# Kernel tuning notes

Measured on AMD Instinct MI355X. Metric: run time of the kernel, lower is better.

## Reference

```python
import jax, jax.numpy as jnp
import numpy as np

B, N, F = 1024, 256, 8
E = 1024
OUT = 128          # NNConv out-channels (hardcoded in module)
N_DIV = 64         # len(num_actions)
PER = 3            # actions per diverter
FEAT = N * OUT     # feature_size() = num_nodes * 128


def setup_inputs() -> dict:
    key = jax.random.key(0)
    ks = jax.random.split(key, 20)
    s = lambda *sh: 0.02
    return {
        "x": jax.random.normal(ks[0], (B, N, F), jnp.float32),
        "edge_index": jax.random.randint(ks[1], (2, E), 0, N, jnp.int64),
        # edge-MLP nn1: Linear(1,64) -> ReLU -> Linear(64, F*OUT)
        "w1": jax.random.normal(ks[2], (1, 64), jnp.float32) * 0.1,
        "b1": jnp.zeros((64,), jnp.float32),
        "w2": jax.random.normal(ks[3], (64, F * OUT), jnp.float32) * 0.02,
        "b2": jnp.zeros((F * OUT,), jnp.float32),
        # NNConv root weight + bias
        "root_w": jax.random.normal(ks[4], (F, OUT), jnp.float32) * 0.1,
        "conv_b": jnp.zeros((OUT,), jnp.float32),
        # dueling heads
        "adv_w": jax.random.normal(ks[5], (FEAT, N_DIV * PER), jnp.float32) * 0.005,
        "adv_b": jnp.zeros((N_DIV * PER,), jnp.float32),
        "v1w": jax.random.normal(ks[6], (FEAT, 64), jnp.float32) * 0.005,
        "v1b": jnp.zeros((64,), jnp.float32),
        "v2w": jax.random.normal(ks[7], (64, 64), jnp.float32) * 0.1,
        "v2b": jnp.zeros((64,), jnp.float32),
        "v3w": jax.random.normal(ks[8], (64, N_DIV), jnp.float32) * 0.1,
        "v3b": jnp.zeros((N_DIV,), jnp.float32),
    }


def reference(x, edge_index, w1, b1, w2, b2, root_w, conv_b,
              adv_w, adv_b, v1w, v1b, v2w, v2b, v3w, v3b):
    b, n, f = x.shape
    out_c = root_w.shape[1]
    n_div = v3w.shape[1]
    flat = x.reshape(b * n, f)                              # [B*N, F]
    e = edge_index.shape[1]
    # edge_attr = ones -> edge MLP produces per-edge weight matrix theta
    ea = jnp.ones((e, 1), x.dtype)
    h = jax.nn.relu(ea @ w1 + b1)
    theta = (h @ w2 + b2).reshape(e, f, out_c)              # [E, F, OUT]
    src, tgt = edge_index[0], edge_index[1]
    # gather source feats -> per-edge matmul -> scatter-add at targets
    msg = jnp.einsum('ef,efo->eo', flat[src], theta)        # [E, OUT]
    agg = jnp.zeros((b * n, out_c), x.dtype).at[tgt].add(msg)
    conv = agg + flat @ root_w + conv_b                      # NNConv root + bias
    feat = jax.nn.relu(conv).reshape(b, -1)                  # [B, N*OUT]
    adv = jax.nn.relu(feat @ adv_w + adv_b).reshape(b, n_div, -1)
    val = jax.nn.relu(feat @ v1w + v1b)
    val = jax.nn.relu(val @ v2w + v2b)
    val = val @ v3w + v3b                                    # [B, n_div]
    return val[..., None] + adv - adv.mean(-1, keepdims=True)
```

## Files before the change

kernel.cpp:

```cpp
#include <hip/hip_runtime.h>

#define Bsz 1024
#define Nn 256
#define Fdim 8
#define Eedge 1024
#define OUTC 128
#define CADV 192
#define CTOT 256
#define Ktot 32768
#define ASTR 40
#define XSTR 24

typedef __attribute__((ext_vector_type(8))) short short8;
typedef __attribute__((ext_vector_type(4))) float float4v;

static __device__ inline unsigned short f2bf(float f) {
  union { float f; unsigned u; } v; v.f = f;
  unsigned r = v.u + 0x7FFFu + ((v.u >> 16) & 1u);
  return (unsigned short)(r >> 16);
}
static __device__ inline float bf2f(unsigned short h) {
  union { unsigned u; float f; } v; v.u = ((unsigned)h) << 16;
  return v.f;
}
static __device__ inline uint4 pack8(const unsigned short* b) {
  uint4 v;
  v.x = (unsigned)b[0] | ((unsigned)b[1] << 16);
  v.y = (unsigned)b[2] | ((unsigned)b[3] << 16);
  v.z = (unsigned)b[4] | ((unsigned)b[5] << 16);
  v.w = (unsigned)b[6] | ((unsigned)b[7] << 16);
  return v;
}
static __device__ inline unsigned cvtpk(float a, float b) {
  unsigned r;
  asm("v_cvt_pk_bf16_f32 %0, %1, %2" : "=v"(r) : "v"(a), "v"(b));
  return r;
}
static __device__ inline float hi_of(unsigned p)  {
  union { unsigned u; float f; } v; v.u = p << 16; return v.f;
}
static __device__ inline float hi2_of(unsigned p) {
  union { unsigned u; float f; } v; v.u = p & 0xFFFF0000u; return v.f;
}

__global__ __launch_bounds__(256) void prep_feat_kernel(
    const float* __restrict__ x, const int* __restrict__ ei,
    const float* __restrict__ w1, const float* __restrict__ b1,
    const float* __restrict__ w2, const float* __restrict__ b2,
    const float* __restrict__ rootw, const float* __restrict__ convb,
    const float* __restrict__ advw, const float* __restrict__ v1w,
    unsigned short* __restrict__ wt, unsigned short* __restrict__ feat0)
{
  __shared__ __align__(16) char smem[20480];
  int bid = blockIdx.x, t = threadIdx.x;

  if (bid < 16) {
    float* fs   = (float*)smem;
    float* h_s  = fs;
    float* rw_s = fs + 64;
    float* th_s = fs + 128;
    float* pt_s = fs + 192;
    float* S_s  = fs + 448;
    int*   flag = (int*)(fs + 2496);
    int obase = bid * 8;

    if (t < 64) {
      h_s[t]  = fmaxf(w1[t] + b1[t], 0.f);
      rw_s[t] = rootw[(t >> 3) * OUTC + obase + (t & 7)];
    }
    for (int i = t; i < Nn * Fdim; i += 256) S_s[i] = 0.f;
    if (t == 0) {
      int z = 0;
      for (int i = 1; i < 16; i += 2) z |= ei[i];
      *flag = (z == 0);
    }
    __syncthreads();
    int is64 = *flag;

    {
      int l = t & 63, g = t >> 6;
      int c = (l >> 3) * 128 + obase + (l & 7);
      float p = 0.f;
#pragma unroll
      for (int j = 0; j < 16; ++j)
        p += h_s[g * 16 + j] * w2[(size_t)(g * 16 + j) * 1024 + c];
      pt_s[t] = p;
    }
    int srcs[4], tgts[4];
#pragma unroll
    for (int q = 0; q < 4; ++q) {
      int e = t + q * 256;
      if (is64) { srcs[q] = ei[2 * e]; tgts[q] = ei[2 * (Eedge + e)]; }
      else      { srcs[q] = ei[e];     tgts[q] = ei[Eedge + e]; }
      srcs[q] &= 255; tgts[q] &= 255;
    }
    __syncthreads();
    if (t < 64) {
      int c = (t >> 3) * 128 + obase + (t & 7);
      th_s[t] = b2[c] + pt_s[t] + pt_s[t + 64] + pt_s[t + 128] + pt_s[t + 192];
    }
#pragma unroll
    for (int q = 0; q < 4; ++q) {
      const float* xp = x + srcs[q] * Fdim;
#pragma unroll
      for (int f = 0; f < Fdim; ++f)
        atomicAdd(&S_s[tgts[q] * Fdim + f], xp[f]);
    }
    __syncthreads();
    {
      int n = t;
      const float* xp = x + n * Fdim;
      float4 xa = *(const float4*)xp;
      float4 xb = *(const float4*)(xp + 4);
      float xv[8] = {xa.x, xa.y, xa.z, xa.w, xb.x, xb.y, xb.z, xb.w};
      float sv[8];
#pragma unroll
      for (int f = 0; f < 8; ++f) sv[f] = S_s[n * Fdim + f];
      unsigned short buf[8];
#pragma unroll
      for (int oi = 0; oi < 8; ++oi) {
        float z = convb[obase + oi];
#pragma unroll
        for (int f = 0; f < 8; ++f)
          z += xv[f] * rw_s[f * 8 + oi] + sv[f] * th_s[f * 8 + oi];
        buf[oi] = f2bf(fmaxf(z, 0.f));
      }
      *(uint4*)(feat0 + (size_t)n * OUTC + obase) = pack8(buf);
    }
  } else {
    unsigned short* st = (unsigned short*)smem;
    int kt = bid - 16, c = t;
    const float* src; int stride, col;
    if (c < CADV) { src = advw; stride = CADV; col = c; }
    else          { src = v1w;  stride = 64;   col = c - CADV; }
    float v[32];
#pragma unroll
    for (int i = 0; i < 32; ++i)
      v[i] = src[(size_t)(kt * 32 + i) * stride + col];
    unsigned pk[16];
#pragma unroll
    for (int i = 0; i < 16; ++i) pk[i] = cvtpk(v[2 * i], v[2 * i + 1]);
#pragma unroll
    for (int p = 0; p < 4; ++p) {
      uint4 w4; w4.x = pk[p * 4]; w4.y = pk[p * 4 + 1];
      w4.z = pk[p * 4 + 2]; w4.w = pk[p * 4 + 3];
      *(uint4*)(st + c * ASTR + p * 8) = w4;
    }
    __syncthreads();
    uint4* dst = (uint4*)(wt + (size_t)kt * (CTOT * 32));
    for (int r = 0; r < 4; ++r) {
      int s = r * 256 + c;
      dst[s] = *(const uint4*)(st + (s >> 2) * ASTR + (s & 3) * 8);
    }
  }
}

__global__ __launch_bounds__(512, 2) void gemm_mfma(
    const float* __restrict__ x, const unsigned short* __restrict__ wt,
    const float* __restrict__ rootw, const float* __restrict__ convb,
    const unsigned short* __restrict__ feat0, float* __restrict__ part,
    int iters, int ns)
{
  __shared__ short a_s[2][64 * ASTR];
  __shared__ short b_s[2][256 * ASTR];
  __shared__ short x_s[2][64 * XSTR];
  __shared__ short rw_s[128 * XSTR];
  __shared__ float convb_s[128];
  int t = threadIdx.x;
  int ch = blockIdx.x;
  int mb = blockIdx.y;
  int wave = t >> 6, lane = t & 63;
  int wm = wave >> 2, wn = wave & 3;
  int lm = lane & 15, lq = lane >> 4;

  float4v acc[2][4];
#pragma unroll
  for (int i = 0; i < 2; ++i)
#pragma unroll
    for (int j = 0; j < 4; ++j) acc[i][j] = (float4v)0.f;

  int kt0 = ch * iters;
  int iters4 = iters >> 2;
  int n0 = ch * iters4;
  int wr0 = (t >> 2) * ASTR + (t & 3) * 8;
  int u1 = t + 512;
  int wr1 = (u1 >> 2) * ASTR + (u1 & 3) * 8;
  int grow = (wave & 3) * 16 + lm;
  int gtt  = wave >> 2;

  if (t < 128) {
    float wv[8];
#pragma unroll
    for (int f = 0; f < 8; ++f) wv[f] = rootw[f * OUTC + t];
    unsigned ph[4];
#pragma unroll
    for (int i = 0; i < 4; ++i) ph[i] = cvtpk(wv[2 * i], wv[2 * i + 1]);
    float wl[8];
#pragma unroll
    for (int i = 0; i < 4; ++i) {
      wl[2 * i]     = wv[2 * i]     - hi_of(ph[i]);
      wl[2 * i + 1] = wv[2 * i + 1] - hi2_of(ph[i]);
    }
    unsigned pl[4];
#pragma unroll
    for (int i = 0; i < 4; ++i) pl[i] = cvtpk(wl[2 * i], wl[2 * i + 1]);
    uint4 wh4; wh4.x = ph[0]; wh4.y = ph[1]; wh4.z = ph[2]; wh4.w = ph[3];
    uint4 wl4; wl4.x = pl[0]; wl4.y = pl[1]; wl4.z = pl[2]; wl4.w = pl[3];
    *(uint4*)(rw_s + t * XSTR)     = wh4;
    *(uint4*)(rw_s + t * XSTR + 8) = wl4;
    convb_s[t] = convb[t];
  }
  int xr = (t & 127) >> 1, xh = t & 1;
  const float* xgb = x + ((size_t)(mb * 64 + xr) * Nn) * Fdim + xh * 4;
  if (t < 128) {
    float4 xv = *(const float4*)(xgb + (size_t)n0 * Fdim);
    uint2 dh, dl;
    dh.x = cvtpk(xv.x, xv.y);
    dh.y = cvtpk(xv.z, xv.w);
    dl.x = cvtpk(xv.x - hi_of(dh.x), xv.y - hi2_of(dh.x));
    dl.y = cvtpk(xv.z - hi_of(dh.y), xv.w - hi2_of(dh.y));
    *(uint2*)(x_s[0] + xr * XSTR + xh * 4)     = dh;
    *(uint2*)(x_s[0] + xr * XSTR + 8 + xh * 4) = dl;
  }
  __syncthreads();

  {
    short8 xf = (short8)0;
    if (lq == 0 || lq == 2) xf = *(const short8*)(x_s[0] + grow * XSTR);
    else if (lq == 1)       xf = *(const short8*)(x_s[0] + grow * XSTR + 8);
    int ot = gtt;
    short8 wf = (short8)0;
    if (lq <= 1)      wf = *(const short8*)(rw_s + (ot * 16 + lm) * XSTR);
    else if (lq == 2) wf = *(const short8*)(rw_s + (ot * 16 + lm) * XSTR + 8);
    float4v c = __builtin_amdgcn_mfma_f32_16x16x32_bf16(wf, xf, (float4v)0.f, 0, 0, 0);
    int o0 = ot * 16 + lq * 4;
    float4 cb = *(const float4*)(convb_s + o0);
    unsigned d0 = cvtpk(fmaxf(c[0] + cb.x, 0.f), fmaxf(c[1] + cb.y, 0.f));
    unsigned d1 = cvtpk(fmaxf(c[2] + cb.z, 0.f), fmaxf(c[3] + cb.w, 0.f));
    if (mb == 0 && grow == 0) {
      const unsigned* f0p = (const unsigned*)(feat0 + ((size_t)n0 * OUTC + o0));
      d0 = f0p[0]; d1 = f0p[1];
    }
    uint2 dd; dd.x = d0; dd.y = d1;
    *(uint2*)(a_s[0] + grow * ASTR + gtt * 16 + lq * 4) = dd;
  }

  const uint4* gB = (const uint4*)wt + (size_t)kt0 * 1024;
  uint4 vb0 = gB[t], vb1 = gB[t + 512];
  float4 xpf = {0.f, 0.f, 0.f, 0.f};

  for (int kk = 0; kk < iters; ++kk) {
    int g = kk & 3, grp = kk >> 2;
    short* bb = b_s[kk & 1];
    *(uint4*)(bb + wr0) = vb0;
    *(uint4*)(bb + wr1) = vb1;
    if (g == 0 && grp + 1 < iters4 && t < 128)
      xpf = *(const float4*)(xgb + (size_t)(n0 + grp + 1) * Fdim);
    if (g == 3 && grp + 1 < iters4 && t < 128) {
      uint2 dh, dl;
      dh.x = cvtpk(xpf.x, xpf.y);
      dh.y = cvtpk(xpf.z, xpf.w);
      dl.x = cvtpk(xpf.x - hi_of(dh.x), xpf.y - hi2_of(dh.x));
      dl.y = cvtpk(xpf.z - hi_of(dh.y), xpf.w - hi2_of(dh.y));
      short* xd = x_s[(grp + 1) & 1];
      *(uint2*)(xd + xr * XSTR + xh * 4)     = dh;
      *(uint2*)(xd + xr * XSTR + 8 + xh * 4) = dl;
    }
    if (kk + 1 < iters) {
      const uint4* gB2 = (const uint4*)wt + (size_t)(kt0 + kk + 1) * 1024;
      vb0 = gB2[t]; vb1 = gB2[t + 512];
    }
    __syncthreads();

    short* ab = a_s[kk & 1];
    short8 aF[2];
#pragma unroll
    for (int i = 0; i < 2; ++i)
      aF[i] = *(const short8*)(ab + (wm * 32 + i * 16 + lm) * ASTR + lq * 8);
#pragma unroll
    for (int j = 0; j < 4; ++j) {
      short8 bF = *(const short8*)(bb + (wn * 64 + j * 16 + lm) * ASTR + lq * 8);
#pragma unroll
      for (int i = 0; i < 2; ++i)
        acc[i][j] = __builtin_amdgcn_mfma_f32_16x16x32_bf16(bF, aF[i], acc[i][j], 0, 0, 0);
    }

    if (kk + 1 < iters) {
      int kn = kk + 1;
      int g2 = kn & 3, grp2 = kn >> 2;
      const short* xs = x_s[grp2 & 1];
      int node2 = n0 + grp2;
      short* ad = a_s[kn & 1];
      short8 xf = (short8)0;
      if (lq == 0 || lq == 2) xf = *(const short8*)(xs + grow * XSTR);
      else if (lq == 1)       xf = *(const short8*)(xs + grow * XSTR + 8);
      int ot = g2 * 2 + gtt;
      short8 wf = (short8)0;
      if (lq <= 1)      wf = *(const short8*)(rw_s + (ot * 16 + lm) * XSTR);
      else if (lq == 2) wf = *(const short8*)(rw_s + (ot * 16 + lm) * XSTR + 8);
      float4v c = __builtin_amdgcn_mfma_f32_16x16x32_bf16(wf, xf, (float4v)0.f, 0, 0, 0);
      int o0 = ot * 16 + lq * 4;
      float4 cb = *(const float4*)(convb_s + o0);
      unsigned d0 = cvtpk(fmaxf(c[0] + cb.x, 0.f), fmaxf(c[1] + cb.y, 0.f));
      unsigned d1 = cvtpk(fmaxf(c[2] + cb.z, 0.f), fmaxf(c[3] + cb.w, 0.f));
      if (mb == 0 && grow == 0) {
        const unsigned* f0p = (const unsigned*)(feat0 + ((size_t)node2 * OUTC + o0));
        d0 = f0p[0]; d1 = f0p[1];
      }
      uint2 dd; dd.x = d0; dd.y = d1;
      *(uint2*)(ad + grow * ASTR + gtt * 16 + lq * 4) = dd;
    }
  }

  float* pb = part + ((size_t)(mb * 64) * ns + ch) * CTOT;
#pragma unroll
  for (int i = 0; i < 2; ++i) {
    int m = wm * 32 + i * 16 + lm;
#pragma unroll
    for (int j = 0; j < 4; ++j) {
      int c = wn * 64 + j * 16 + lq * 4;
      *(float4v*)(pb + (size_t)m * ns * CTOT + c) = acc[i][j];
    }
  }
}

__global__ __launch_bounds__(256) void final_kernel(
    const float* __restrict__ part, int ns,
    const float* __restrict__ advb, const float* __restrict__ v1b,
    const float* __restrict__ v2w, const float* __restrict__ v2b,
    const float* __restrict__ v3w, const float* __restrict__ v3b,
    float* __restrict__ out)
{
  __shared__ float4v red_s[4][64];
  __shared__ float adv_s[CADV];
  __shared__ float v1_s[64];
  __shared__ float val2_s[64];
  __shared__ float val3_s[64];
  int b = blockIdx.x, t = threadIdx.x;
  int q = t & 63, r0 = t >> 6;
  const float4v* p4 = (const float4v*)(part + (size_t)b * ns * CTOT);
  float4v s4 = (float4v)0.f;
  for (int i = r0; i < ns; i += 4) s4 += p4[i * 64 + q];
  red_s[r0][q] = s4;
  __syncthreads();
  float s;
  {
    const float* rs = (const float*)red_s;
    s = rs[t] + rs[256 + t] + rs[512 + t] + rs[768 + t];
  }
  if (t < CADV) adv_s[t] = fmaxf(s + advb[t], 0.f);
  else          v1_s[t - CADV] = fmaxf(s + v1b[t - CADV], 0.f);
  __syncthreads();
  if (t < 64) {
    float a = v2b[t];
#pragma unroll
    for (int i = 0; i < 64; ++i) a += v1_s[i] * v2w[i * 64 + t];
    val2_s[t] = fmaxf(a, 0.f);
  }
  __syncthreads();
  if (t < 64) {
    float a = v3b[t];
#pragma unroll
    for (int j = 0; j < 64; ++j) a += val2_s[j] * v3w[j * 64 + t];
    val3_s[t] = a;
  }
  __syncthreads();
  if (t < CADV) {
    int d = t / 3;
    float mean = (adv_s[d * 3] + adv_s[d * 3 + 1] + adv_s[d * 3 + 2]) * (1.f / 3.f);
    out[(size_t)b * CADV + t] = val3_s[d] + adv_s[t] - mean;
  }
}

extern "C" void kernel_launch(void* const* d_in, const int* in_sizes, int n_in,
                              void* d_out, int out_size, void* d_ws, size_t ws_size,
                              hipStream_t stream)
{
  (void)in_sizes; (void)n_in; (void)out_size;
  const float* x     = (const float*)d_in[0];
  const int*   ei    = (const int*)d_in[1];
  const float* w1    = (const float*)d_in[2];
  const float* b1    = (const float*)d_in[3];
  const float* w2    = (const float*)d_in[4];
  const float* b2    = (const float*)d_in[5];
  const float* rootw = (const float*)d_in[6];
  const float* convb = (const float*)d_in[7];
  const float* advw  = (const float*)d_in[8];
  const float* advb  = (const float*)d_in[9];
  const float* v1w   = (const float*)d_in[10];
  const float* v1b   = (const float*)d_in[11];
  const float* v2w   = (const float*)d_in[12];
  const float* v2b   = (const float*)d_in[13];
  const float* v3w   = (const float*)d_in[14];
  const float* v3b   = (const float*)d_in[15];
  float* out = (float*)d_out;

  const size_t f0B = 131072;
  const size_t wtB = (size_t)Ktot * CTOT * 2;

  int NS = 32;
  while (NS > 8 && f0B + wtB + (size_t)NS * Bsz * CTOT * 4 > ws_size)
    NS >>= 1;

  unsigned short* feat0 = (unsigned short*)d_ws;
  unsigned short* wtp   = (unsigned short*)((char*)d_ws + f0B);
  float* part = (float*)((char*)d_ws + f0B + wtB);

  prep_feat_kernel<<<1040, 256, 0, stream>>>(x, ei, w1, b1, w2, b2, rootw,
                                             convb, advw, v1w, wtp, feat0);
  gemm_mfma<<<dim3(NS, 16), 512, 0, stream>>>(x, wtp, rootw, convb, feat0, part,
                                              1024 / NS, NS);
  final_kernel<<<Bsz, 256, 0, stream>>>(part, NS, advb, v1b, v2w, v2b, v3w, v3b, out);
}
```

Measured before the change: 165.5 us.

## Split GEMM output columns across a grid z-dimension and build x fragments in registers

The GEMM's 256 output columns are split into two halves handled by separate blocks (grid z=2). This halves the B tile in shared memory and the accumulators per thread, and launch bounds are raised to 4 blocks per CU for higher occupancy. The x hi/lo bf16 fragments are now built directly in registers from global loads instead of being staged through shared memory. The catch is that the A-side work (x conversion and the root-weight MFMA) is duplicated across the two column halves, and each block does less MFMA work per barrier.

```diff
diff --git a/kernel.cpp b/kernel.cpp
--- a/kernel.cpp
+++ b/kernel.cpp
@@ -19,10 +19,6 @@
   unsigned r = v.u + 0x7FFFu + ((v.u >> 16) & 1u);
   return (unsigned short)(r >> 16);
 }
-static __device__ inline float bf2f(unsigned short h) {
-  union { unsigned u; float f; } v; v.u = ((unsigned)h) << 16;
-  return v.f;
-}
 static __device__ inline uint4 pack8(const unsigned short* b) {
   uint4 v;
   v.x = (unsigned)b[0] | ((unsigned)b[1] << 16);
@@ -41,6 +37,19 @@
 }
 static __device__ inline float hi2_of(unsigned p) {
   union { unsigned u; float f; } v; v.u = p & 0xFFFF0000u; return v.f;
+}
+static __device__ inline short8 make_frag(float4 a, float4 b, int lq) {
+  union { unsigned u[4]; short8 s; } uu;
+  unsigned h0 = cvtpk(a.x, a.y), h1 = cvtpk(a.z, a.w);
+  unsigned h2 = cvtpk(b.x, b.y), h3 = cvtpk(b.z, b.w);
+  uu.u[0] = h0; uu.u[1] = h1; uu.u[2] = h2; uu.u[3] = h3;
+  if (lq == 1) {
+    uu.u[0] = cvtpk(a.x - hi_of(h0), a.y - hi2_of(h0));
+    uu.u[1] = cvtpk(a.z - hi_of(h1), a.w - hi2_of(h1));
+    uu.u[2] = cvtpk(b.x - hi_of(h2), b.y - hi2_of(h2));
+    uu.u[3] = cvtpk(b.z - hi_of(h3), b.w - hi2_of(h3));
+  }
+  return uu.s;
 }
 
 __global__ __launch_bounds__(256) void prep_feat_kernel(
@@ -155,36 +164,34 @@
   }
 }
 
-__global__ __launch_bounds__(512, 2) void gemm_mfma(
+__global__ __launch_bounds__(512, 4) void gemm_mfma(
     const float* __restrict__ x, const unsigned short* __restrict__ wt,
     const float* __restrict__ rootw, const float* __restrict__ convb,
     const unsigned short* __restrict__ feat0, float* __restrict__ part,
     int iters, int ns)
 {
   __shared__ short a_s[2][64 * ASTR];
-  __shared__ short b_s[2][256 * ASTR];
-  __shared__ short x_s[2][64 * XSTR];
+  __shared__ short b_s[2][128 * ASTR];
   __shared__ short rw_s[128 * XSTR];
   __shared__ float convb_s[128];
   int t = threadIdx.x;
   int ch = blockIdx.x;
   int mb = blockIdx.y;
+  int nc = blockIdx.z;
   int wave = t >> 6, lane = t & 63;
   int wm = wave >> 2, wn = wave & 3;
   int lm = lane & 15, lq = lane >> 4;
 
-  float4v acc[2][4];
+  float4v acc[2][2];
 #pragma unroll
   for (int i = 0; i < 2; ++i)
 #pragma unroll
-    for (int j = 0; j < 4; ++j) acc[i][j] = (float4v)0.f;
+    for (int j = 0; j < 2; ++j) acc[i][j] = (float4v)0.f;
 
   int kt0 = ch * iters;
   int iters4 = iters >> 2;
   int n0 = ch * iters4;
   int wr0 = (t >> 2) * ASTR + (t & 3) * 8;
-  int u1 = t + 512;
-  int wr1 = (u1 >> 2) * ASTR + (u1 & 3) * 8;
   int grow = (wave & 3) * 16 + lm;
   int gtt  = wave >> 2;
 
@@ -210,29 +217,24 @@
     *(uint4*)(rw_s + t * XSTR + 8) = wl4;
     convb_s[t] = convb[t];
   }
-  int xr = (t & 127) >> 1, xh = t & 1;
-  const float* xgb = x + ((size_t)(mb * 64 + xr) * Nn) * Fdim + xh * 4;
-  if (t < 128) {
-    float4 xv = *(const float4*)(xgb + (size_t)n0 * Fdim);
-    uint2 dh, dl;
-    dh.x = cvtpk(xv.x, xv.y);
-    dh.y = cvtpk(xv.z, xv.w);
-    dl.x = cvtpk(xv.x - hi_of(dh.x), xv.y - hi2_of(dh.x));
-    dl.y = cvtpk(xv.z - hi_of(dh.y), xv.w - hi2_of(dh.y));
-    *(uint2*)(x_s[0] + xr * XSTR + xh * 4)     = dh;
-    *(uint2*)(x_s[0] + xr * XSTR + 8 + xh * 4) = dl;
+  const float* xrow = x + ((size_t)(mb * 64 + grow) * Nn) * Fdim;
+  float4 xa0 = *(const float4*)(xrow + (size_t)n0 * Fdim);
+  float4 xb0 = *(const float4*)(xrow + (size_t)n0 * Fdim + 4);
+  short8 xf_cur = make_frag(xa0, xb0, lq);
+  short8 xf_next = xf_cur;
+  float4 xpa = xa0, xpb = xb0;
+  if (iters4 > 1) {
+    xpa = *(const float4*)(xrow + (size_t)(n0 + 1) * Fdim);
+    xpb = *(const float4*)(xrow + (size_t)(n0 + 1) * Fdim + 4);
   }
   __syncthreads();
 
   {
-    short8 xf = (short8)0;
-    if (lq == 0 || lq == 2) xf = *(const short8*)(x_s[0] + grow * XSTR);
-    else if (lq == 1)       xf = *(const short8*)(x_s[0] + grow * XSTR + 8);
     int ot = gtt;
     short8 wf = (short8)0;
     if (lq <= 1)      wf = *(const short8*)(rw_s + (ot * 16 + lm) * XSTR);
     else if (lq == 2) wf = *(const short8*)(rw_s + (ot * 16 + lm) * XSTR + 8);
-    float4v c = __builtin_amdgcn_mfma_f32_16x16x32_bf16(wf, xf, (float4v)0.f, 0, 0, 0);
+    float4v c = __builtin_amdgcn_mfma_f32_16x16x32_bf16(wf, xf_cur, (float4v)0.f, 0, 0, 0);
     int o0 = ot * 16 + lq * 4;
     float4 cb = *(const float4*)(convb_s + o0);
     unsigned d0 = cvtpk(fmaxf(c[0] + cb.x, 0.f), fmaxf(c[1] + cb.y, 0.f));
@@ -245,31 +247,21 @@
     *(uint2*)(a_s[0] + grow * ASTR + gtt * 16 + lq * 4) = dd;
   }
 
-  const uint4* gB = (const uint4*)wt + (size_t)kt0 * 1024;
-  uint4 vb0 = gB[t], vb1 = gB[t + 512];
-  float4 xpf = {0.f, 0.f, 0.f, 0.f};
+  const uint4* gB = (const uint4*)wt;
+  uint4 vb0 = gB[(size_t)kt0 * 1024 + nc * 512 + t];
 
   for (int kk = 0; kk < iters; ++kk) {
     int g = kk & 3, grp = kk >> 2;
     short* bb = b_s[kk & 1];
     *(uint4*)(bb + wr0) = vb0;
-    *(uint4*)(bb + wr1) = vb1;
-    if (g == 0 && grp + 1 < iters4 && t < 128)
-      xpf = *(const float4*)(xgb + (size_t)(n0 + grp + 1) * Fdim);
-    if (g == 3 && grp + 1 < iters4 && t < 128) {
-      uint2 dh, dl;
-      dh.x = cvtpk(xpf.x, xpf.y);
-      dh.y = cvtpk(xpf.z, xpf.w);
-      dl.x = cvtpk(xpf.x - hi_of(dh.x), xpf.y - hi2_of(dh.x));
-      dl.y = cvtpk(xpf.z - hi_of(dh.y), xpf.w - hi2_of(dh.y));
-      short* xd = x_s[(grp + 1) & 1];
-      *(uint2*)(xd + xr * XSTR + xh * 4)     = dh;
-      *(uint2*)(xd + xr * XSTR + 8 + xh * 4) = dl;
-    }
-    if (kk + 1 < iters) {
-      const uint4* gB2 = (const uint4*)wt + (size_t)(kt0 + kk + 1) * 1024;
-      vb0 = gB2[t]; vb1 = gB2[t + 512];
-    }
+    if (g == 0 && grp + 1 < iters4) {
+      xpa = *(const float4*)(xrow + (size_t)(n0 + grp + 1) * Fdim);
+      xpb = *(const float4*)(xrow + (size_t)(n0 + grp + 1) * Fdim + 4);
+    }
+    if (g == 3 && grp + 1 < iters4)
+      xf_next = make_frag(xpa, xpb, lq);
+    if (kk + 1 < iters)
+      vb0 = gB[(size_t)(kt0 + kk + 1) * 1024 + nc * 512 + t];
     __syncthreads();
 
     short* ab = a_s[kk & 1];
@@ -278,8 +270,8 @@
     for (int i = 0; i < 2; ++i)
       aF[i] = *(const short8*)(ab + (wm * 32 + i * 16 + lm) * ASTR + lq * 8);
 #pragma unroll
-    for (int j = 0; j < 4; ++j) {
-      short8 bF = *(const short8*)(bb + (wn * 64 + j * 16 + lm) * ASTR + lq * 8);
+    for (int j = 0; j < 2; ++j) {
+      short8 bF = *(const short8*)(bb + (wn * 32 + j * 16 + lm) * ASTR + lq * 8);
 #pragma unroll
       for (int i = 0; i < 2; ++i)
         acc[i][j] = __builtin_amdgcn_mfma_f32_16x16x32_bf16(bF, aF[i], acc[i][j], 0, 0, 0);
@@ -288,12 +280,9 @@
     if (kk + 1 < iters) {
       int kn = kk + 1;
       int g2 = kn & 3, grp2 = kn >> 2;
-      const short* xs = x_s[grp2 & 1];
       int node2 = n0 + grp2;
       short* ad = a_s[kn & 1];
-      short8 xf = (short8)0;
-      if (lq == 0 || lq == 2) xf = *(const short8*)(xs + grow * XSTR);
-      else if (lq == 1)       xf = *(const short8*)(xs + grow * XSTR + 8);
+      short8 xf = (g == 3) ? xf_next : xf_cur;
       int ot = g2 * 2 + gtt;
       short8 wf = (short8)0;
       if (lq <= 1)      wf = *(const short8*)(rw_s + (ot * 16 + lm) * XSTR);
@@ -309,16 +298,17 @@
       }
       uint2 dd; dd.x = d0; dd.y = d1;
       *(uint2*)(ad + grow * ASTR + gtt * 16 + lq * 4) = dd;
-    }
-  }
-
-  float* pb = part + ((size_t)(mb * 64) * ns + ch) * CTOT;
+      if (g == 3) xf_cur = xf_next;
+    }
+  }
+
+  float* pb = part + ((size_t)(mb * 64) * ns + ch) * CTOT + nc * 128;
 #pragma unroll
   for (int i = 0; i < 2; ++i) {
     int m = wm * 32 + i * 16 + lm;
 #pragma unroll
-    for (int j = 0; j < 4; ++j) {
-      int c = wn * 64 + j * 16 + lq * 4;
+    for (int j = 0; j < 2; ++j) {
+      int c = wn * 32 + j * 16 + lq * 4;
       *(float4v*)(pb + (size_t)m * ns * CTOT + c) = acc[i][j];
     }
   }
@@ -408,7 +398,7 @@
 
   prep_feat_kernel<<<1040, 256, 0, stream>>>(x, ei, w1, b1, w2, b2, rootw,
                                              convb, advw, v1w, wtp, feat0);
-  gemm_mfma<<<dim3(NS, 16), 512, 0, stream>>>(x, wtp, rootw, convb, feat0, part,
-                                              1024 / NS, NS);
+  gemm_mfma<<<dim3(NS, 16, 2), 512, 0, stream>>>(x, wtp, rootw, convb, feat0,
+                                                 part, 1024 / NS, NS);
   final_kernel<<<Bsz, 256, 0, stream>>>(part, NS, advb, v1b, v2w, v2b, v3w, v3b, out);
 }
```

Result: slower. 182.1 us (+10.0%).
